# Kernel optimization log

Hardware: AMD Instinct MI355X
Metric: run time of the kernel (lower is better)

## Reference

```python
import jax, jax.numpy as jnp
import numpy as np

N = 100000      # nodes
E = 1600000     # edges (no self-loops; self-loops added in reference, per PyG defaults)
IN = 128        # in_size
HID = 32        # hide_size (per-head channels)
HEADS = 4       # n_heads
OUT = 128       # out_size
NEG_SLOPE = 0.2 # PyG GATConv default negative_slope


def setup_inputs() -> dict:
    key = jax.random.key(0)
    ks = jax.random.split(key, 8)
    x = jax.random.normal(ks[0], (N, IN), jnp.float32)
    # edges guaranteed non-self-loop: dst = (src + offset) % N with offset in [1, N)
    src = jax.random.randint(ks[1], (E,), 0, N, dtype=jnp.int32)
    off = jax.random.randint(ks[2], (E,), 1, N, dtype=jnp.int32)
    dst = ((src + off) % N).astype(jnp.int32)
    edge_index = jnp.stack([src, dst])  # [2, E]
    edge_weight = jax.random.uniform(ks[3], (E,), jnp.float32)
    glorot = lambda k, shape, fan: jax.random.normal(k, shape, jnp.float32) / np.sqrt(fan).astype(np.float32)
    W_gat = glorot(ks[4], (IN, HEADS * HID), IN)      # GATConv lin weight (bias=False)
    att_src = glorot(ks[5], (HEADS, HID), HID)        # GATConv att_src
    att_dst = glorot(ks[6], (HEADS, HID), HID)        # GATConv att_dst
    W_gcn = glorot(ks[7], (HEADS * HID, OUT), HEADS * HID)  # GCNConv weight (bias=False)
    return {"x": x, "edge_index": edge_index, "edge_weight": edge_weight,
            "W_gat": W_gat, "att_src": att_src, "att_dst": att_dst, "W_gcn": W_gcn}


def reference(x, edge_index, edge_weight, W_gat, att_src, att_dst, W_gcn):
    n = x.shape[0]
    loop = jnp.arange(n, dtype=edge_index.dtype)
    src = jnp.concatenate([edge_index[0], loop])  # add self-loops (PyG default)
    dst = jnp.concatenate([edge_index[1], loop])

    # ---- GATConv (concat heads, bias=False) ----
    xp = (x @ W_gat).reshape(n, HEADS, HID)                  # [N,H,C]
    a_s = jnp.einsum('nhc,hc->nh', xp, att_src)              # [N,H]
    a_d = jnp.einsum('nhc,hc->nh', xp, att_dst)
    alpha = jax.nn.leaky_relu(a_s[src] + a_d[dst], NEG_SLOPE)  # [E+N,H]
    m = jax.ops.segment_max(alpha, dst, num_segments=n)     # segment softmax over incoming edges
    e = jnp.exp(alpha - m[dst])
    denom = jax.ops.segment_sum(e, dst, num_segments=n)
    a = e / denom[dst]                                       # [E+N,H]
    y_gat = jax.ops.segment_sum(xp[src] * a[:, :, None], dst, num_segments=n)
    y_gat = y_gat.reshape(n, HEADS * HID)                    # [N, H*C]

    # ---- GCNConv (normalize=True, bias=False), self-loop weight = 1 ----
    ew = jnp.concatenate([edge_weight, jnp.ones((n,), edge_weight.dtype)])
    deg = jax.ops.segment_sum(ew, dst, num_segments=n)
    dinv = jnp.where(deg > 0, jax.lax.rsqrt(deg), 0.0)
    norm = dinv[src] * ew * dinv[dst]                        # [E+N]
    h = y_gat @ W_gcn                                        # [N, OUT]
    out = jax.ops.segment_sum(h[src] * norm[:, None], dst, num_segments=n)
    return out
```

## Files before the change

kernel.cpp:

```cpp
#include <hip/hip_runtime.h>

#define NN 100000
#define EE 1600000
#define TOT (EE + NN)
#define NEG 0.2f
#define FILL_BLKS ((TOT + 255) / 256)
#define GEMM_BLKS ((NN + 63) / 64)

typedef unsigned int uint;
typedef unsigned short ushort;
typedef unsigned char uchar;

__device__ inline ushort f2bf(float f) {
    uint u = __float_as_uint(f);
    return (ushort)((u + 0x7fff + ((u >> 16) & 1)) >> 16);
}

__device__ inline int imin(int a, int b) { return a < b ? a : b; }


__global__ void k_hist(const int* __restrict__ dst, int* counts, uchar* rank) {
    int e = blockIdx.x * 256 + threadIdx.x;
    if (e < EE) {
        int r = atomicAdd(&counts[dst[e]], 1);
        rank[e] = (uchar)r;
    }
}

__global__ void k_scan1(const int* __restrict__ counts, int* row_off, int* partial) {
    __shared__ int sm[256];
    int i = blockIdx.x * 256 + threadIdx.x;
    int v = (i < NN) ? counts[i] + 1 : 0;
    sm[threadIdx.x] = v;
    __syncthreads();
    for (int off = 1; off < 256; off <<= 1) {
        int t = (threadIdx.x >= off) ? sm[threadIdx.x - off] : 0;
        __syncthreads();
        sm[threadIdx.x] += t;
        __syncthreads();
    }
    if (i < NN) row_off[i] = sm[threadIdx.x] - v;
    if (threadIdx.x == 255) partial[blockIdx.x] = sm[255];
}

__global__ void k_scan2(int* partial, int nb) {
    __shared__ int sm[512];
    int t = threadIdx.x;
    int v = (t < nb) ? partial[t] : 0;
    sm[t] = v;
    __syncthreads();
    for (int off = 1; off < 512; off <<= 1) {
        int x = (t >= off) ? sm[t - off] : 0;
        __syncthreads();
        sm[t] += x;
        __syncthreads();
    }
    if (t < nb) partial[t] = sm[t] - v;
}

__global__ void k_scan3(int* row_off, const int* __restrict__ partial) {
    int i = blockIdx.x * 256 + threadIdx.x;
    if (i < NN) row_off[i] += partial[blockIdx.x];
    if (i == 0) row_off[NN] = TOT;
}


__launch_bounds__(256) __global__
void k_fill_gemm(const int* __restrict__ src, const int* __restrict__ dst,
                 const float* __restrict__ ew, const int* __restrict__ row_off,
                 const int* __restrict__ counts, const uchar* __restrict__ rank,
                 long long* __restrict__ csr,
                 const float* __restrict__ A, const float* __restrict__ W,
                 ushort* __restrict__ C16,
                 const float* __restrict__ att_s, const float* __restrict__ att_d,
                 float* __restrict__ a_s, float* __restrict__ a_d) {
    if (blockIdx.x < FILL_BLKS) {
        int e = blockIdx.x * 256 + threadIdx.x;
        if (e >= TOT) return;
        int node, s, r; float w;
        if (e < EE) { node = dst[e]; s = src[e]; w = ew[e]; r = rank[e]; }
        else        { node = e - EE; s = node;  w = 1.0f;  r = counts[node]; }
        int pos = row_off[node] + r;
        long long rec = (long long)(uint)s | ((long long)__float_as_uint(w) << 32);
        __builtin_nontemporal_store(rec, csr + pos);
        return;
    }
    int bid = blockIdx.x - FILL_BLKS;
    int lane = threadIdx.x & 63;
    int cg = __builtin_amdgcn_readfirstlane(threadIdx.x >> 6);
    int row = bid * 64 + lane;
    bool valid = row < NN;
    if (!valid) row = NN - 1;
    const float* __restrict__ a = A + (size_t)row * 128;
    const float* __restrict__ w = W + cg * 32;
    float acc[32];
#pragma unroll
    for (int c = 0; c < 32; ++c) acc[c] = 0.f;
    for (int k = 0; k < 128; k += 4) {
        float4 xv = *(const float4*)(a + k);
        float xs[4] = {xv.x, xv.y, xv.z, xv.w};
#pragma unroll
        for (int kk = 0; kk < 4; ++kk) {
            const float* wr = w + (k + kk) * 128;
            float xk = xs[kk];
#pragma unroll
            for (int c = 0; c < 32; ++c) acc[c] = fmaf(xk, wr[c], acc[c]);
        }
    }
    if (valid) {
        ushort* o = C16 + (size_t)row * 128 + cg * 32;
#pragma unroll
        for (int c = 0; c < 32; c += 8) {
            uint4 p;
            p.x = (uint)f2bf(acc[c+0]) | ((uint)f2bf(acc[c+1]) << 16);
            p.y = (uint)f2bf(acc[c+2]) | ((uint)f2bf(acc[c+3]) << 16);
            p.z = (uint)f2bf(acc[c+4]) | ((uint)f2bf(acc[c+5]) << 16);
            p.w = (uint)f2bf(acc[c+6]) | ((uint)f2bf(acc[c+7]) << 16);
            *(uint4*)(o + c) = p;
        }
        const float* as = att_s + cg * 32;
        const float* ad = att_d + cg * 32;
        float s0 = 0.f, s1 = 0.f;
#pragma unroll
        for (int c = 0; c < 32; ++c) {
            s0 = fmaf(acc[c], as[c], s0);
            s1 = fmaf(acc[c], ad[c], s1);
        }
        a_s[row * 4 + cg] = s0;
        a_d[row * 4 + cg] = s1;
    }
}


__launch_bounds__(256) __global__
void k_gemm2(const float* __restrict__ A, const float* __restrict__ W,
             ushort* __restrict__ C16, const float* __restrict__ dscale) {
    int lane = threadIdx.x & 63;
    int cg = __builtin_amdgcn_readfirstlane(threadIdx.x >> 6);
    int row = blockIdx.x * 64 + lane;
    bool valid = row < NN;
    if (!valid) row = NN - 1;
    const float* __restrict__ a = A + (size_t)row * 128;
    const float* __restrict__ w = W + cg * 32;
    float acc[32];
#pragma unroll
    for (int c = 0; c < 32; ++c) acc[c] = 0.f;
    for (int k = 0; k < 128; k += 4) {
        float4 xv = *(const float4*)(a + k);
        float xs[4] = {xv.x, xv.y, xv.z, xv.w};
#pragma unroll
        for (int kk = 0; kk < 4; ++kk) {
            const float* wr = w + (k + kk) * 128;
            float xk = xs[kk];
#pragma unroll
            for (int c = 0; c < 32; ++c) acc[c] = fmaf(xk, wr[c], acc[c]);
        }
    }
    if (valid) {
        float sc = dscale[row];
        ushort* o = C16 + (size_t)row * 128 + cg * 32;
#pragma unroll
        for (int c = 0; c < 32; c += 8) {
            uint4 p;
            p.x = (uint)f2bf(acc[c+0]*sc) | ((uint)f2bf(acc[c+1]*sc) << 16);
            p.y = (uint)f2bf(acc[c+2]*sc) | ((uint)f2bf(acc[c+3]*sc) << 16);
            p.z = (uint)f2bf(acc[c+4]*sc) | ((uint)f2bf(acc[c+5]*sc) << 16);
            p.w = (uint)f2bf(acc[c+6]*sc) | ((uint)f2bf(acc[c+7]*sc) << 16);
            *(uint4*)(o + c) = p;
        }
    }
}


__launch_bounds__(256) __global__
void k_gat(const int* __restrict__ row_off, const int2* __restrict__ csr,
           const float* __restrict__ a_s, const float* __restrict__ a_d,
           const ushort* __restrict__ xp16,
           float* __restrict__ ygat, float* __restrict__ dinv) {
    int lane = threadIdx.x & 63;
    int node = blockIdx.x * 4 + (threadIdx.x >> 6);
    int base = row_off[node], end = row_off[node + 1];
    int grp = lane >> 4, sl = lane & 15, h2 = sl >> 2;
    float adh = a_d[node * 4 + h2];
    float acc[8];
#pragma unroll
    for (int j = 0; j < 8; ++j) acc[j] = 0.f;
    float den = 0.f, wsum = 0.f;
    int na = end - 1;
    int i0 = base + grp;
    int2 eA = csr[imin(i0, na)];
    int2 eB = csr[imin(i0 + 4, na)];
    for (int i = i0; i < end; i += 8) {
        int2 eA2 = csr[imin(i + 8,  na)];
        int2 eB2 = csr[imin(i + 12, na)];
        uint4 qA = *(const uint4*)(xp16 + (size_t)eA.x * 128 + sl * 8);
        uint4 qB = *(const uint4*)(xp16 + (size_t)eB.x * 128 + sl * 8);
        float alA = a_s[eA.x * 4 + h2] + adh;
        alA = alA > 0.f ? alA : NEG * alA;
        float awA = __expf(alA);
        float awB = 0.f, wB = 0.f;
        if (i + 4 < end) {
            float alB = a_s[eB.x * 4 + h2] + adh;
            alB = alB > 0.f ? alB : NEG * alB;
            awB = __expf(alB);
            wB = __int_as_float(eB.y);
        }
        den  += awA + awB;
        wsum += __int_as_float(eA.y) + wB;
        acc[0] = fmaf(awA, __uint_as_float(qA.x << 16),         fmaf(awB, __uint_as_float(qB.x << 16),         acc[0]));
        acc[1] = fmaf(awA, __uint_as_float(qA.x & 0xffff0000u), fmaf(awB, __uint_as_float(qB.x & 0xffff0000u), acc[1]));
        acc[2] = fmaf(awA, __uint_as_float(qA.y << 16),         fmaf(awB, __uint_as_float(qB.y << 16),         acc[2]));
        acc[3] = fmaf(awA, __uint_as_float(qA.y & 0xffff0000u), fmaf(awB, __uint_as_float(qB.y & 0xffff0000u), acc[3]));
        acc[4] = fmaf(awA, __uint_as_float(qA.z << 16),         fmaf(awB, __uint_as_float(qB.z << 16),         acc[4]));
        acc[5] = fmaf(awA, __uint_as_float(qA.z & 0xffff0000u), fmaf(awB, __uint_as_float(qB.z & 0xffff0000u), acc[5]));
        acc[6] = fmaf(awA, __uint_as_float(qA.w << 16),         fmaf(awB, __uint_as_float(qB.w << 16),         acc[6]));
        acc[7] = fmaf(awA, __uint_as_float(qA.w & 0xffff0000u), fmaf(awB, __uint_as_float(qB.w & 0xffff0000u), acc[7]));
        eA = eA2; eB = eB2;
    }
#pragma unroll
    for (int j = 0; j < 8; ++j) {
        acc[j] += __shfl_xor(acc[j], 16);
        acc[j] += __shfl_xor(acc[j], 32);
    }
    den  += __shfl_xor(den, 16);   den  += __shfl_xor(den, 32);
    wsum += __shfl_xor(wsum, 16);  wsum += __shfl_xor(wsum, 32);
    if (grp == 0) {
        float il = 1.f / den;
        float* o = ygat + (size_t)node * 128 + sl * 8;
        *(float4*)(o)     = make_float4(acc[0]*il, acc[1]*il, acc[2]*il, acc[3]*il);
        *(float4*)(o + 4) = make_float4(acc[4]*il, acc[5]*il, acc[6]*il, acc[7]*il);
        if (sl == 0) dinv[node] = rsqrtf(wsum);
    }
}


__launch_bounds__(256) __global__
void k_gcn(const int* __restrict__ row_off, const int2* __restrict__ csr,
           const float* __restrict__ dinv, const ushort* __restrict__ h16,
           float* __restrict__ out) {
    int lane = threadIdx.x & 63;
    int node = blockIdx.x * 4 + (threadIdx.x >> 6);
    int base = row_off[node], end = row_off[node + 1];
    float dn = dinv[node];
    int grp = lane >> 4, sl = lane & 15;
    float acc[8];
#pragma unroll
    for (int j = 0; j < 8; ++j) acc[j] = 0.f;
    int na = end - 1;
    int i0 = base + grp;
    int2 eA = csr[imin(i0, na)];
    int2 eB = csr[imin(i0 + 4, na)];
    for (int i = i0; i < end; i += 8) {
        int2 eA2 = csr[imin(i + 8,  na)];
        int2 eB2 = csr[imin(i + 12, na)];
        uint4 qA = *(const uint4*)(h16 + (size_t)eA.x * 128 + sl * 8);
        uint4 qB = *(const uint4*)(h16 + (size_t)eB.x * 128 + sl * 8);
        float cA = __int_as_float(eA.y) * dn;
        float cB = (i + 4 < end) ? __int_as_float(eB.y) * dn : 0.f;
        acc[0] = fmaf(cA, __uint_as_float(qA.x << 16),         fmaf(cB, __uint_as_float(qB.x << 16),         acc[0]));
        acc[1] = fmaf(cA, __uint_as_float(qA.x & 0xffff0000u), fmaf(cB, __uint_as_float(qB.x & 0xffff0000u), acc[1]));
        acc[2] = fmaf(cA, __uint_as_float(qA.y << 16),         fmaf(cB, __uint_as_float(qB.y << 16),         acc[2]));
        acc[3] = fmaf(cA, __uint_as_float(qA.y & 0xffff0000u), fmaf(cB, __uint_as_float(qB.y & 0xffff0000u), acc[3]));
        acc[4] = fmaf(cA, __uint_as_float(qA.z << 16),         fmaf(cB, __uint_as_float(qB.z << 16),         acc[4]));
        acc[5] = fmaf(cA, __uint_as_float(qA.z & 0xffff0000u), fmaf(cB, __uint_as_float(qB.z & 0xffff0000u), acc[5]));
        acc[6] = fmaf(cA, __uint_as_float(qA.w << 16),         fmaf(cB, __uint_as_float(qB.w << 16),         acc[6]));
        acc[7] = fmaf(cA, __uint_as_float(qA.w & 0xffff0000u), fmaf(cB, __uint_as_float(qB.w & 0xffff0000u), acc[7]));
        eA = eA2; eB = eB2;
    }
#pragma unroll
    for (int j = 0; j < 8; ++j) {
        acc[j] += __shfl_xor(acc[j], 16);
        acc[j] += __shfl_xor(acc[j], 32);
    }
    if (grp == 0) {
        float* o = out + (size_t)node * 128 + sl * 8;
        *(float4*)(o)     = make_float4(acc[0], acc[1], acc[2], acc[3]);
        *(float4*)(o + 4) = make_float4(acc[4], acc[5], acc[6], acc[7]);
    }
}


extern "C" void kernel_launch(void* const* d_in, const int* in_sizes, int n_in,
                              void* d_out, int out_size, void* d_ws, size_t ws_size,
                              hipStream_t stream) {
    const float* x    = (const float*)d_in[0];
    const int*   ei   = (const int*)  d_in[1];
    const float* ew   = (const float*)d_in[2];
    const float* Wg   = (const float*)d_in[3];
    const float* atts = (const float*)d_in[4];
    const float* attd = (const float*)d_in[5];
    const float* Wc   = (const float*)d_in[6];
    float* out = (float*)d_out;

    float* ygat  = (float*)d_ws;
    float* a_s   = ygat + 12800000;
    float* a_d   = a_s + 400000;
    float* dinvp = a_d + 400000;
    int* row_off = (int*)(dinvp + 100000);
    int* counts  = row_off + 100004;
    int* partial = counts + 100000;
    long long* csr = (long long*)(partial + 1024);
    ushort* xp16 = (ushort*)(csr + 1700000);
    ushort* h16  = xp16 + 12800000;
    uchar* rank  = (uchar*)h16;

    const int* srcv = ei;
    const int* dstv = ei + EE;

    hipMemsetAsync(counts, 0, NN * sizeof(int), stream);
    k_hist <<<(EE + 255) / 256, 256, 0, stream>>>(dstv, counts, rank);
    k_scan1<<<391, 256, 0, stream>>>(counts, row_off, partial);
    k_scan2<<<1, 512, 0, stream>>>(partial, 391);
    k_scan3<<<391, 256, 0, stream>>>(row_off, partial);
    k_fill_gemm<<<FILL_BLKS + GEMM_BLKS, 256, 0, stream>>>(
        srcv, dstv, ew, row_off, counts, rank, csr,
        x, Wg, xp16, atts, attd, a_s, a_d);
    k_gat  <<<NN / 4, 256, 0, stream>>>(row_off, (const int2*)csr, a_s, a_d, xp16,
                                        ygat, dinvp);
    k_gemm2<<<GEMM_BLKS, 256, 0, stream>>>(ygat, Wc, h16, dinvp);
    k_gcn  <<<NN / 4, 256, 0, stream>>>(row_off, (const int2*)csr, dinvp, h16, out);
}
```

Before: 557.6 us.

## Build CSR via two-level bucket sort instead of global atomic histogram

Replaces per-node global atomic histogram, three-kernel scan and scatter fill with a coarse bucket count, block-local binning into 256 destination buckets with coalesced writes, and a per-bucket fine sort in shared memory fused with the first GEMM. This targets contention on global atomics and scattered CSR writes. It also adds a software prefetch of the next input float4 in both GEMM loops. The extra pass over edges and the intermediate binned buffer add traffic, and the CSR order within a node now depends on atomic ordering.

```diff
diff --git a/kernel.cpp b/kernel.cpp
--- a/kernel.cpp
+++ b/kernel.cpp
@@ -4,12 +4,14 @@
 #define EE 1600000
 #define TOT (EE + NN)
 #define NEG 0.2f
-#define FILL_BLKS ((TOT + 255) / 256)
+#define NB 256
+#define CH 391
+#define TILE 4096
+#define NTILES ((EE + TILE - 1) / TILE)
 #define GEMM_BLKS ((NN + 63) / 64)
 
 typedef unsigned int uint;
 typedef unsigned short ushort;
-typedef unsigned char uchar;
 
 __device__ inline ushort f2bf(float f) {
     uint u = __float_as_uint(f);
@@ -19,73 +21,117 @@
 __device__ inline int imin(int a, int b) { return a < b ? a : b; }
 
 
-__global__ void k_hist(const int* __restrict__ dst, int* counts, uchar* rank) {
-    int e = blockIdx.x * 256 + threadIdx.x;
-    if (e < EE) {
-        int r = atomicAdd(&counts[dst[e]], 1);
-        rank[e] = (uchar)r;
-    }
-}
-
-__global__ void k_scan1(const int* __restrict__ counts, int* row_off, int* partial) {
-    __shared__ int sm[256];
-    int i = blockIdx.x * 256 + threadIdx.x;
-    int v = (i < NN) ? counts[i] + 1 : 0;
-    sm[threadIdx.x] = v;
-    __syncthreads();
-    for (int off = 1; off < 256; off <<= 1) {
-        int t = (threadIdx.x >= off) ? sm[threadIdx.x - off] : 0;
-        __syncthreads();
-        sm[threadIdx.x] += t;
-        __syncthreads();
-    }
-    if (i < NN) row_off[i] = sm[threadIdx.x] - v;
-    if (threadIdx.x == 255) partial[blockIdx.x] = sm[255];
-}
-
-__global__ void k_scan2(int* partial, int nb) {
-    __shared__ int sm[512];
+__launch_bounds__(256) __global__
+void k_bcount(const int* __restrict__ dst, int* __restrict__ bcnt) {
+    __shared__ int h[NB];
     int t = threadIdx.x;
-    int v = (t < nb) ? partial[t] : 0;
-    sm[t] = v;
-    __syncthreads();
-    for (int off = 1; off < 512; off <<= 1) {
-        int x = (t >= off) ? sm[t - off] : 0;
-        __syncthreads();
-        sm[t] += x;
-        __syncthreads();
-    }
-    if (t < nb) partial[t] = sm[t] - v;
-}
-
-__global__ void k_scan3(int* row_off, const int* __restrict__ partial) {
-    int i = blockIdx.x * 256 + threadIdx.x;
-    if (i < NN) row_off[i] += partial[blockIdx.x];
-    if (i == 0) row_off[NN] = TOT;
-}
-
-
-__launch_bounds__(256) __global__
-void k_fill_gemm(const int* __restrict__ src, const int* __restrict__ dst,
-                 const float* __restrict__ ew, const int* __restrict__ row_off,
-                 const int* __restrict__ counts, const uchar* __restrict__ rank,
-                 long long* __restrict__ csr,
-                 const float* __restrict__ A, const float* __restrict__ W,
-                 ushort* __restrict__ C16,
-                 const float* __restrict__ att_s, const float* __restrict__ att_d,
-                 float* __restrict__ a_s, float* __restrict__ a_d) {
-    if (blockIdx.x < FILL_BLKS) {
-        int e = blockIdx.x * 256 + threadIdx.x;
-        if (e >= TOT) return;
-        int node, s, r; float w;
-        if (e < EE) { node = dst[e]; s = src[e]; w = ew[e]; r = rank[e]; }
-        else        { node = e - EE; s = node;  w = 1.0f;  r = counts[node]; }
-        int pos = row_off[node] + r;
-        long long rec = (long long)(uint)s | ((long long)__float_as_uint(w) << 32);
-        __builtin_nontemporal_store(rec, csr + pos);
-        return;
-    }
-    int bid = blockIdx.x - FILL_BLKS;
+    h[t] = 0;
+    __syncthreads();
+    int base = blockIdx.x * TILE;
+#pragma unroll
+    for (int r = 0; r < 16; ++r) {
+        int e = base + r * 256 + t;
+        if (e < EE) atomicAdd(&h[dst[e] / CH], 1);
+    }
+    __syncthreads();
+    if (h[t]) atomicAdd(&bcnt[t], h[t]);
+}
+
+
+__launch_bounds__(NB) __global__
+void k_bprefix(const int* __restrict__ bcnt, int* __restrict__ boff,
+               int* __restrict__ bcsr, int* __restrict__ bfill) {
+    __shared__ int s1[NB], s2[NB];
+    int t = threadIdx.x;
+    int c = bcnt[t];
+    int nb0 = t * CH;
+    int nib = imin(nb0 + CH, NN) - nb0;
+    s1[t] = c; s2[t] = c + nib;
+    __syncthreads();
+    for (int off = 1; off < NB; off <<= 1) {
+        int a = (t >= off) ? s1[t - off] : 0;
+        int b = (t >= off) ? s2[t - off] : 0;
+        __syncthreads();
+        s1[t] += a; s2[t] += b;
+        __syncthreads();
+    }
+    int ex = s1[t] - c;
+    boff[t] = ex;
+    bfill[t] = ex;
+    bcsr[t] = s2[t] - (c + nib);
+    if (t == NB - 1) boff[NB] = EE;
+}
+
+
+__launch_bounds__(256) __global__
+void k_bin(const int* __restrict__ src, const int* __restrict__ dst,
+           const float* __restrict__ ew, int* __restrict__ bfill,
+           long long* __restrict__ binned) {
+    __shared__ long long recs[TILE];
+    __shared__ ushort    bkt[TILE];
+    __shared__ int hist[NB], eoff[NB], gbase[NB];
+    int t = threadIdx.x;
+    hist[t] = 0;
+    __syncthreads();
+    int base = blockIdx.x * TILE;
+    int cnt = imin(TILE, EE - base);
+    long long rec[16]; int binfo[16];
+#pragma unroll
+    for (int r = 0; r < 16; ++r) {
+        int i = r * 256 + t;
+        if (i < cnt) {
+            int e = base + i;
+            int s = src[e], d = dst[e];
+            float w = ew[e];
+            int b = d / CH;
+            int ldst = d - b * CH;
+            int rk = atomicAdd(&hist[b], 1);
+            rec[r] = (long long)(uint)(s | (ldst << 17)) |
+                     ((long long)__float_as_uint(w) << 32);
+            binfo[r] = b | (rk << 8);
+        }
+    }
+    __syncthreads();
+    int c = hist[t];
+    eoff[t] = c;
+    __syncthreads();
+    for (int off = 1; off < NB; off <<= 1) {
+        int a = (t >= off) ? eoff[t - off] : 0;
+        __syncthreads();
+        eoff[t] += a;
+        __syncthreads();
+    }
+    int ex = eoff[t] - c;
+    gbase[t] = atomicAdd(&bfill[t], c);
+    eoff[t] = ex;
+    __syncthreads();
+#pragma unroll
+    for (int r = 0; r < 16; ++r) {
+        int i = r * 256 + t;
+        if (i < cnt) {
+            int b = binfo[r] & 255, rk = binfo[r] >> 8;
+            int slot = eoff[b] + rk;
+            recs[slot] = rec[r];
+            bkt[slot] = (ushort)b;
+        }
+    }
+    __syncthreads();
+#pragma unroll
+    for (int r = 0; r < 16; ++r) {
+        int i = r * 256 + t;
+        if (i < cnt) {
+            int b = bkt[i];
+            binned[gbase[b] + (i - eoff[b])] = recs[i];
+        }
+    }
+}
+
+
+__device__ __forceinline__ void gemm1_body(
+    int bid, const float* __restrict__ A, const float* __restrict__ W,
+    ushort* __restrict__ C16, const float* __restrict__ att_s,
+    const float* __restrict__ att_d, float* __restrict__ a_s,
+    float* __restrict__ a_d) {
     int lane = threadIdx.x & 63;
     int cg = __builtin_amdgcn_readfirstlane(threadIdx.x >> 6);
     int row = bid * 64 + lane;
@@ -96,8 +142,10 @@
     float acc[32];
 #pragma unroll
     for (int c = 0; c < 32; ++c) acc[c] = 0.f;
+    float4 xv = *(const float4*)(a);
     for (int k = 0; k < 128; k += 4) {
-        float4 xv = *(const float4*)(a + k);
+        float4 nx = xv;
+        if (k < 124) nx = *(const float4*)(a + k + 4);
         float xs[4] = {xv.x, xv.y, xv.z, xv.w};
 #pragma unroll
         for (int kk = 0; kk < 4; ++kk) {
@@ -106,6 +154,7 @@
 #pragma unroll
             for (int c = 0; c < 32; ++c) acc[c] = fmaf(xk, wr[c], acc[c]);
         }
+        xv = nx;
     }
     if (valid) {
         ushort* o = C16 + (size_t)row * 128 + cg * 32;
@@ -128,6 +177,73 @@
         }
         a_s[row * 4 + cg] = s0;
         a_d[row * 4 + cg] = s1;
+    }
+}
+
+
+__launch_bounds__(256) __global__
+void k_fine_gemm(const long long* __restrict__ binned, const int* __restrict__ boff,
+                 const int* __restrict__ bcsr, int* __restrict__ row_off,
+                 long long* __restrict__ csr,
+                 const float* __restrict__ A, const float* __restrict__ W,
+                 ushort* __restrict__ C16, const float* __restrict__ att_s,
+                 const float* __restrict__ att_d, float* __restrict__ a_s,
+                 float* __restrict__ a_d) {
+    if (blockIdx.x >= NB) {
+        gemm1_body(blockIdx.x - NB, A, W, C16, att_s, att_d, a_s, a_d);
+        return;
+    }
+    __shared__ int hist[CH];
+    __shared__ int excl[CH];
+    __shared__ int sc[512];
+    int t = threadIdx.x;
+    int b = blockIdx.x;
+    int e0 = boff[b], e1 = boff[b + 1];
+    int nb0 = b * CH;
+    int nnode = imin(CH, NN - nb0);
+    const int2* __restrict__ bn = (const int2*)binned;
+    hist[t] = 0;
+    if (t + 256 < CH) hist[t + 256] = 0;
+    __syncthreads();
+    for (int i = e0 + t; i < e1; i += 256)
+        atomicAdd(&hist[bn[i].x >> 17], 1);
+    __syncthreads();
+    int v0 = (t < nnode) ? hist[t] + 1 : 0;
+    int v1 = (t + 256 < nnode) ? hist[t + 256] + 1 : 0;
+    sc[t] = v0; sc[t + 256] = v1;
+    __syncthreads();
+    for (int off = 1; off < 512; off <<= 1) {
+        int a0 = (t >= off) ? sc[t - off] : 0;
+        int a1 = (t + 256 >= off) ? sc[t + 256 - off] : 0;
+        __syncthreads();
+        sc[t] += a0; sc[t + 256] += a1;
+        __syncthreads();
+    }
+    int csr0 = bcsr[b];
+    if (t < nnode) {
+        excl[t] = csr0 + sc[t] - v0;
+        row_off[nb0 + t] = excl[t];
+    }
+    if (t + 256 < nnode) {
+        excl[t + 256] = csr0 + sc[t + 256] - v1;
+        row_off[nb0 + t + 256] = excl[t + 256];
+    }
+    if (b == 0 && t == 0) row_off[NN] = TOT;
+    hist[t] = 0;
+    if (t + 256 < CH) hist[t + 256] = 0;
+    __syncthreads();
+    for (int i = e0 + t; i < e1; i += 256) {
+        int2 r = bn[i];
+        int ld = r.x >> 17;
+        int rk = atomicAdd(&hist[ld], 1);
+        long long rec = (long long)(uint)(r.x & 0x1FFFF) |
+                        ((long long)(uint)r.y << 32);
+        csr[excl[ld] + rk] = rec;
+    }
+    __syncthreads();
+    for (int i = t; i < nnode; i += 256) {
+        int n = nb0 + i;
+        csr[excl[i] + hist[i]] = (long long)(uint)n | (0x3F800000LL << 32);
     }
 }
 
@@ -145,8 +261,10 @@
     float acc[32];
 #pragma unroll
     for (int c = 0; c < 32; ++c) acc[c] = 0.f;
+    float4 xv = *(const float4*)(a);
     for (int k = 0; k < 128; k += 4) {
-        float4 xv = *(const float4*)(a + k);
+        float4 nx = xv;
+        if (k < 124) nx = *(const float4*)(a + k + 4);
         float xs[4] = {xv.x, xv.y, xv.z, xv.w};
 #pragma unroll
         for (int kk = 0; kk < 4; ++kk) {
@@ -155,6 +273,7 @@
 #pragma unroll
             for (int c = 0; c < 32; ++c) acc[c] = fmaf(xk, wr[c], acc[c]);
         }
+        xv = nx;
     }
     if (valid) {
         float sc = dscale[row];
@@ -297,23 +416,24 @@
     float* a_d   = a_s + 400000;
     float* dinvp = a_d + 400000;
     int* row_off = (int*)(dinvp + 100000);
-    int* counts  = row_off + 100004;
-    int* partial = counts + 100000;
-    long long* csr = (long long*)(partial + 1024);
+    int* bcnt    = row_off + 100004;
+    int* boff    = bcnt + NB;
+    int* bcsr    = boff + NB + 1;
+    int* bfill   = bcsr + NB;
+    long long* csr = (long long*)(bfill + NB + 1);
     ushort* xp16 = (ushort*)(csr + 1700000);
     ushort* h16  = xp16 + 12800000;
-    uchar* rank  = (uchar*)h16;
+    long long* binned = (long long*)h16;
 
     const int* srcv = ei;
     const int* dstv = ei + EE;
 
-    hipMemsetAsync(counts, 0, NN * sizeof(int), stream);
-    k_hist <<<(EE + 255) / 256, 256, 0, stream>>>(dstv, counts, rank);
-    k_scan1<<<391, 256, 0, stream>>>(counts, row_off, partial);
-    k_scan2<<<1, 512, 0, stream>>>(partial, 391);
-    k_scan3<<<391, 256, 0, stream>>>(row_off, partial);
-    k_fill_gemm<<<FILL_BLKS + GEMM_BLKS, 256, 0, stream>>>(
-        srcv, dstv, ew, row_off, counts, rank, csr,
+    hipMemsetAsync(bcnt, 0, NB * sizeof(int), stream);
+    k_bcount <<<NTILES, 256, 0, stream>>>(dstv, bcnt);
+    k_bprefix<<<1, NB, 0, stream>>>(bcnt, boff, bcsr, bfill);
+    k_bin    <<<NTILES, 256, 0, stream>>>(srcv, dstv, ew, bfill, binned);
+    k_fine_gemm<<<NB + GEMM_BLKS, 256, 0, stream>>>(
+        binned, boff, bcsr, row_off, csr,
         x, Wg, xp16, atts, attd, a_s, a_d);
     k_gat  <<<NN / 4, 256, 0, stream>>>(row_off, (const int2*)csr, a_s, a_d, xp16,
                                         ygat, dinvp);
```

After: 486.7 us. 12.7% less time.
